# Kernel optimization log

Measured on AMD Instinct MI355X. Metric: run time of the kernel, lower is better.

## Reference

```python
import jax, jax.numpy as jnp
import numpy as np

S = 128      # number of segments
F = 256      # in_features
H = 128      # mlp hidden


def setup_inputs() -> dict:
    key = jax.random.key(0)
    k1, k2, k3 = jax.random.split(key, 3)
    rng = np.random.default_rng(0)
    lengths = rng.integers(1024, 3073, size=S).astype(np.int32)  # ragged segment sizes
    N = int(lengths.sum())  # ~262144 total tokens
    x = jax.random.normal(k1, (N, F), dtype=jnp.float32)
    W1 = jax.random.normal(k2, (F, H), dtype=jnp.float32) * (1.0 / np.sqrt(F))
    b1 = jnp.zeros((H,), dtype=jnp.float32)
    W2 = jax.random.normal(k3, (H, 2), dtype=jnp.float32) * (1.0 / np.sqrt(H))
    b2 = jnp.zeros((2,), dtype=jnp.float32)
    return {"x": x, "lengths": jnp.asarray(lengths), "W1": W1, "b1": b1, "W2": W2, "b2": b2}


def reference(x, lengths, W1, b1, W2, b2):
    N = x.shape[0]
    nseg = lengths.shape[0]
    seg_ids = jnp.repeat(jnp.arange(nseg), lengths, total_repeat_length=N)  # [N]
    offsets = jnp.concatenate([jnp.zeros((1,), lengths.dtype), jnp.cumsum(lengths)[:-1]])
    # position within segment: arange(1, L+1) / L
    pos = (jnp.arange(N) - offsets[seg_ids] + 1).astype(x.dtype)
    Lf = lengths.astype(x.dtype)
    xpos = pos / Lf[seg_ids]  # [N]

    # MLP: Linear -> Tanh -> Linear
    ms = jnp.tanh(x @ W1 + b1) @ W2 + b2  # [N, 2]
    y, z = ms[:, 0], ms[:, 1]

    # per-segment softmax-weighted mean of positions (calc_mean)
    ymax = jax.ops.segment_max(y, seg_ids, num_segments=nseg)
    w = jnp.exp(y - ymax[seg_ids])
    wsum = jax.ops.segment_sum(w, seg_ids, num_segments=nseg)
    means = jax.ops.segment_sum(xpos * w, seg_ids, num_segments=nseg) / wsum  # [S]

    # per-segment softplus(mean(z))
    stds = jax.nn.softplus(jax.ops.segment_sum(z, seg_ids, num_segments=nseg) / Lf)  # [S]

    # normal pdf weights per token
    mu = means[seg_ids]
    sd = stds[seg_ids]
    inv_sqrt_2pi = 1.0 / jnp.sqrt(2.0 * jnp.pi).astype(x.dtype)
    pdf = jnp.exp(-0.5 * ((xpos - mu) / sd) ** 2) * (inv_sqrt_2pi / sd)  # [N]

    # normalize per segment with +0.001 stabilizer
    psum = jax.ops.segment_sum(pdf, seg_ids, num_segments=nseg)
    attn = (pdf / (psum[seg_ids] + 0.001))[:, None]  # [N, 1]

    # attention-weighted sum of features per segment
    out = jax.ops.segment_sum(attn * x, seg_ids, num_segments=nseg)  # [S, F]
    return out, attn
```

## Files before the change

### kernel.cpp

```cpp
#include <hip/hip_runtime.h>
#include <math.h>

#define F 256
#define Hh 128
#define MAXL 3072

typedef short bf16x8 __attribute__((ext_vector_type(8)));
typedef float f32x4 __attribute__((ext_vector_type(4)));
typedef unsigned int uint4v __attribute__((ext_vector_type(4)));

__device__ inline unsigned short f2bf_rne(float f) {
  unsigned u = __float_as_uint(f);
  unsigned r = u + 0x7fff + ((u >> 16) & 1);
  return (unsigned short)(r >> 16);
}
__device__ inline float bf2f(unsigned short h) {
  return __uint_as_float((unsigned)h << 16);
}

__global__ void init_kernel(const int* __restrict__ lengths, int* __restrict__ offsets,
                            float* __restrict__ out, const float* __restrict__ W1,
                            unsigned short* __restrict__ whT, unsigned short* __restrict__ wlT,
                            int S, int outN) {
  int t = blockIdx.x * blockDim.x + threadIdx.x;
  int stride = gridDim.x * blockDim.x;
  for (int i = t; i < outN; i += stride) out[i] = 0.f;
  for (int i = t; i < F * Hh; i += stride) {
    int k = i >> 7, col = i & 127;
    float v = W1[i];
    unsigned short h = f2bf_rne(v);
    unsigned short l = f2bf_rne(v - bf2f(h));
    int dst = (k >> 5) * (128 * 32) + col * 32 + (k & 31);
    whT[dst] = h;
    wlT[dst] = l;
  }
  if (blockIdx.x == 0) {
    __shared__ int buf[256];
    int tid = threadIdx.x;
    int v = (tid < S) ? lengths[tid] : 0;
    buf[tid] = v;
    __syncthreads();
    for (int o = 1; o < 256; o <<= 1) {
      int add = (tid >= o) ? buf[tid - o] : 0;
      __syncthreads();
      buf[tid] += add;
      __syncthreads();
    }
    if (tid < S) offsets[tid] = buf[tid] - v;
    if (tid == S - 1) offsets[S] = buf[tid];
  }
}

__global__ __launch_bounds__(256) void mlp_kernel(
    const float* __restrict__ x,
    const unsigned short* __restrict__ whT, const unsigned short* __restrict__ wlT,
    const float* __restrict__ b1, const float* __restrict__ W2,
    const float* __restrict__ b2, float* __restrict__ yv,
    float* __restrict__ zv, int N) {
  __shared__ float redy[128][2];
  __shared__ float redz[128][2];

  const int t = threadIdx.x;
  const int lane = t & 63;
  const int w = t >> 6;
  const int wr = w >> 1, wc = w & 1;
  const int ln15 = lane & 15, lq = lane >> 4;

  const int row0 = blockIdx.x * 128;

  f32x4 acc[4][4];
#pragma unroll
  for (int i = 0; i < 4; ++i)
#pragma unroll
    for (int j = 0; j < 4; ++j) acc[i][j] = (f32x4){0.f, 0.f, 0.f, 0.f};

  int rowg[4];
  bool rv[4];
#pragma unroll
  for (int rt = 0; rt < 4; ++rt) {
    rowg[rt] = row0 + wr * 64 + rt * 16 + ln15;
    rv[rt] = rowg[rt] < N;
  }
  const int cbase = wc * 64 + ln15;

  for (int kc = 0; kc < 8; ++kc) {
    float4 av0[4], av1[4];
#pragma unroll
    for (int rt = 0; rt < 4; ++rt) {
      av0[rt] = make_float4(0.f, 0.f, 0.f, 0.f);
      av1[rt] = make_float4(0.f, 0.f, 0.f, 0.f);
      if (rv[rt]) {
        const float* p = &x[(size_t)rowg[rt] * F + kc * 32 + lq * 8];
        av0[rt] = *(const float4*)p;
        av1[rt] = *(const float4*)(p + 4);
      }
    }
    bf16x8 bh[4], bl[4];
#pragma unroll
    for (int ct = 0; ct < 4; ++ct) {
      int o = kc * 4096 + (cbase + ct * 16) * 32 + lq * 8;
      bh[ct] = *(const bf16x8*)&whT[o];
      bl[ct] = *(const bf16x8*)&wlT[o];
    }
#pragma unroll
    for (int rt = 0; rt < 4; ++rt) {
      float f[8] = {av0[rt].x, av0[rt].y, av0[rt].z, av0[rt].w,
                    av1[rt].x, av1[rt].y, av1[rt].z, av1[rt].w};
      union { uint4v u; bf16x8 b; } ah, al;
#pragma unroll
      for (int q = 0; q < 4; ++q) {
        unsigned ua = __float_as_uint(f[2 * q]);
        unsigned ub = __float_as_uint(f[2 * q + 1]);
        ah.u[q] = __builtin_amdgcn_perm(ub, ua, 0x07060302u);
        float ra = f[2 * q]     - __uint_as_float(ua & 0xFFFF0000u);
        float rb = f[2 * q + 1] - __uint_as_float(ub & 0xFFFF0000u);
        al.u[q] = __builtin_amdgcn_perm(__float_as_uint(rb), __float_as_uint(ra), 0x07060302u);
      }
#pragma unroll
      for (int ct = 0; ct < 4; ++ct) {
        acc[rt][ct] = __builtin_amdgcn_mfma_f32_16x16x32_bf16(ah.b, bh[ct], acc[rt][ct], 0, 0, 0);
        acc[rt][ct] = __builtin_amdgcn_mfma_f32_16x16x32_bf16(ah.b, bl[ct], acc[rt][ct], 0, 0, 0);
        acc[rt][ct] = __builtin_amdgcn_mfma_f32_16x16x32_bf16(al.b, bh[ct], acc[rt][ct], 0, 0, 0);
      }
    }
  }

  float yp[4][4], zp[4][4];
#pragma unroll
  for (int i = 0; i < 4; ++i)
#pragma unroll
    for (int j = 0; j < 4; ++j) { yp[i][j] = 0.f; zp[i][j] = 0.f; }
#pragma unroll
  for (int ct = 0; ct < 4; ++ct) {
    int c = cbase + ct * 16;
    float b1c = b1[c], wyc = W2[2 * c], wzc = W2[2 * c + 1];
#pragma unroll
    for (int rt = 0; rt < 4; ++rt)
#pragma unroll
      for (int rg = 0; rg < 4; ++rg) {
        float a = acc[rt][ct][rg] + b1c;
        float e = __expf(2.f * a);
        float h = 1.f - __fdividef(2.f, e + 1.f);
        yp[rt][rg] = fmaf(h, wyc, yp[rt][rg]);
        zp[rt][rg] = fmaf(h, wzc, zp[rt][rg]);
      }
  }
#pragma unroll
  for (int rt = 0; rt < 4; ++rt)
#pragma unroll
    for (int rg = 0; rg < 4; ++rg) {
      float vy = yp[rt][rg], vz = zp[rt][rg];
#pragma unroll
      for (int m = 8; m; m >>= 1) {
        vy += __shfl_xor(vy, m);
        vz += __shfl_xor(vz, m);
      }
      if (ln15 == 0) {
        int row = wr * 64 + rt * 16 + lq * 4 + rg;
        redy[row][wc] = vy;
        redz[row][wc] = vz;
      }
    }
  __syncthreads();
  if (t < 128) {
    int g = row0 + t;
    if (g < N) {
      yv[g] = redy[t][0] + redy[t][1] + b2[0];
      zv[g] = redz[t][0] + redz[t][1] + b2[1];
    }
  }
}

__device__ inline float wave_reduce_sum(float v) {
#pragma unroll
  for (int o = 32; o; o >>= 1) v += __shfl_down(v, o);
  return v;
}
__device__ inline float wave_reduce_max(float v) {
#pragma unroll
  for (int o = 32; o; o >>= 1) v = fmaxf(v, __shfl_down(v, o));
  return v;
}

__global__ __launch_bounds__(256) void pool_kernel(
    const float* __restrict__ x,
    const float* __restrict__ yv, const float* __restrict__ zv,
    const int* __restrict__ offsets, const int* __restrict__ lengths,
    float* __restrict__ attn, float* __restrict__ out,
    int nchunks, int S) {
  __shared__ float ybuf[MAXL];
  __shared__ float4 sbuf[4][64];
  __shared__ float redA[4], redB[4], redC[4];

  const int s = S - 1 - blockIdx.y;
  const int c = nchunks - 1 - blockIdx.x;
  const int off = offsets[s], L = lengths[s];
  const int t = threadIdx.x;
  const int lane = t & 63, wid = t >> 6;

  float lmax = -1e30f;
  for (int i = t; i < L; i += 256) {
    float yy = yv[off + i];
    ybuf[i] = yy;
    lmax = fmaxf(lmax, yy);
  }
  lmax = wave_reduce_max(lmax);
  if (lane == 0) redA[wid] = lmax;
  __syncthreads();
  const float ymax = fmaxf(fmaxf(redA[0], redA[1]), fmaxf(redA[2], redA[3]));
  const float invL = 1.f / (float)L;
  __syncthreads();

  float sw = 0.f, smx = 0.f, sz = 0.f;
  for (int i = t; i < L; i += 256) {
    float wgt = __expf(ybuf[i] - ymax);
    float xp = (float)(i + 1) * invL;
    sw += wgt;
    smx = fmaf(xp, wgt, smx);
    sz += zv[off + i];
  }
  sw = wave_reduce_sum(sw);
  smx = wave_reduce_sum(smx);
  sz = wave_reduce_sum(sz);
  if (lane == 0) { redA[wid] = sw; redB[wid] = smx; redC[wid] = sz; }
  __syncthreads();
  const float wsum = (redA[0] + redA[1]) + (redA[2] + redA[3]);
  const float mxs  = (redB[0] + redB[1]) + (redB[2] + redB[3]);
  const float zsum = (redC[0] + redC[1]) + (redC[2] + redC[3]);
  const float mu = mxs / wsum;
  const float tz = zsum * invL;
  const float sd = fmaxf(tz, 0.f) + log1pf(__expf(-fabsf(tz)));
  const float invsd = 1.f / sd;
  const float Cg = 0.3989422804014327f;
  __syncthreads();

  float ps = 0.f;
  for (int i = t; i < L; i += 256) {
    float xp = (float)(i + 1) * invL;
    float u = (xp - mu) * invsd;
    ps += __expf(-0.5f * u * u);
  }
  ps = wave_reduce_sum(ps);
  if (lane == 0) redA[wid] = ps;
  __syncthreads();
  const float psum = ((redA[0] + redA[1]) + (redA[2] + redA[3])) * (Cg * invsd);
  const float scale = (Cg * invsd) / (psum + 0.001f);

  const int i0 = (int)((long long)L * c / nchunks);
  const int i1 = (int)((long long)L * (c + 1) / nchunks);
  for (int i = i0 + t; i < i1; i += 256) {
    float xp = (float)(i + 1) * invL;
    float u = (xp - mu) * invsd;
    attn[off + i] = __expf(-0.5f * u * u) * scale;
  }

  float4 a0 = make_float4(0.f, 0.f, 0.f, 0.f);
  float4 a1 = make_float4(0.f, 0.f, 0.f, 0.f);
  int i = i1 - 1 - wid;
  for (; i - 4 >= i0; i -= 8) {
    float xpa = (float)(i + 1) * invL;
    float ua = (xpa - mu) * invsd;
    float w0 = __expf(-0.5f * ua * ua) * scale;
    float xpb = (float)(i - 3) * invL;
    float ub = (xpb - mu) * invsd;
    float w1 = __expf(-0.5f * ub * ub) * scale;
    float4 v0 = *(const float4*)&x[(size_t)(off + i) * F + lane * 4];
    float4 v1 = *(const float4*)&x[(size_t)(off + i - 4) * F + lane * 4];
    a0.x = fmaf(w0, v0.x, a0.x); a0.y = fmaf(w0, v0.y, a0.y);
    a0.z = fmaf(w0, v0.z, a0.z); a0.w = fmaf(w0, v0.w, a0.w);
    a1.x = fmaf(w1, v1.x, a1.x); a1.y = fmaf(w1, v1.y, a1.y);
    a1.z = fmaf(w1, v1.z, a1.z); a1.w = fmaf(w1, v1.w, a1.w);
  }
  if (i >= i0) {
    float xpa = (float)(i + 1) * invL;
    float ua = (xpa - mu) * invsd;
    float w0 = __expf(-0.5f * ua * ua) * scale;
    float4 v0 = *(const float4*)&x[(size_t)(off + i) * F + lane * 4];
    a0.x = fmaf(w0, v0.x, a0.x); a0.y = fmaf(w0, v0.y, a0.y);
    a0.z = fmaf(w0, v0.z, a0.z); a0.w = fmaf(w0, v0.w, a0.w);
  }
  a0.x += a1.x; a0.y += a1.y; a0.z += a1.z; a0.w += a1.w;
  sbuf[wid][lane] = a0;
  __syncthreads();
  if (wid == 0) {
    float4 r0 = sbuf[0][lane], r1 = sbuf[1][lane];
    float4 r2 = sbuf[2][lane], r3 = sbuf[3][lane];
    float rx = (r0.x + r1.x) + (r2.x + r3.x);
    float ry = (r0.y + r1.y) + (r2.y + r3.y);
    float rz = (r0.z + r1.z) + (r2.z + r3.z);
    float rw = (r0.w + r1.w) + (r2.w + r3.w);
    float* o = &out[s * F + lane * 4];
    atomicAdd(o + 0, rx);
    atomicAdd(o + 1, ry);
    atomicAdd(o + 2, rz);
    atomicAdd(o + 3, rw);
  }
}

extern "C" void kernel_launch(void* const* d_in, const int* in_sizes, int n_in,
                              void* d_out, int out_size, void* d_ws, size_t ws_size,
                              hipStream_t stream) {
  const float* x      = (const float*)d_in[0];
  const int* lengths  = (const int*)d_in[1];
  const float* W1     = (const float*)d_in[2];
  const float* b1     = (const float*)d_in[3];
  const float* W2     = (const float*)d_in[4];
  const float* b2     = (const float*)d_in[5];
  const int S = in_sizes[1];
  const int N = in_sizes[0] / F;

  float* out  = (float*)d_out;
  float* attn = out + (size_t)S * F;

  int*   offsets = (int*)d_ws;
  float* yv = (float*)d_ws + 512;
  float* zv = yv + N;
  unsigned short* whT = (unsigned short*)(zv + N);
  unsigned short* wlT = whT + F * Hh;

  init_kernel<<<64, 256, 0, stream>>>(lengths, offsets, out, W1, whT, wlT, S, S * F);
  mlp_kernel<<<(N + 127) / 128, 256, 0, stream>>>(x, whT, wlT, b1, W2, b2, yv, zv, N);
  pool_kernel<<<dim3(32, S), 256, 0, stream>>>(x, yv, zv, offsets, lengths, attn, out, 32, S);
}
```

Baseline: 459.9 us.

## Halve MLP row tile, double-buffer x loads, and cut pool chunks

Result: slower. 482.6 us (+4.9%).

```diff
diff --git a/kernel.cpp b/kernel.cpp
--- a/kernel.cpp
+++ b/kernel.cpp
@@ -51,14 +51,26 @@
   }
 }
 
+#define LOADX(B, KC) do {                                             \
+    _Pragma("unroll")                                                 \
+    for (int rt = 0; rt < 2; ++rt) {                                  \
+      a0[B][rt] = make_float4(0.f, 0.f, 0.f, 0.f);                    \
+      a1[B][rt] = make_float4(0.f, 0.f, 0.f, 0.f);                    \
+      if (rv[rt]) {                                                   \
+        a0[B][rt] = *(const float4*)(xb[rt] + (KC) * 32);             \
+        a1[B][rt] = *(const float4*)(xb[rt] + (KC) * 32 + 4);         \
+      }                                                               \
+    }                                                                 \
+  } while (0)
+
 __global__ __launch_bounds__(256) void mlp_kernel(
     const float* __restrict__ x,
     const unsigned short* __restrict__ whT, const unsigned short* __restrict__ wlT,
     const float* __restrict__ b1, const float* __restrict__ W2,
     const float* __restrict__ b2, float* __restrict__ yv,
     float* __restrict__ zv, int N) {
-  __shared__ float redy[128][2];
-  __shared__ float redz[128][2];
+  __shared__ float redy[64][2];
+  __shared__ float redz[64][2];
 
   const int t = threadIdx.x;
   const int lane = t & 63;
@@ -66,46 +78,43 @@
   const int wr = w >> 1, wc = w & 1;
   const int ln15 = lane & 15, lq = lane >> 4;
 
-  const int row0 = blockIdx.x * 128;
-
-  f32x4 acc[4][4];
-#pragma unroll
-  for (int i = 0; i < 4; ++i)
+  const int row0 = blockIdx.x * 64;
+
+  f32x4 acc[2][4];
+#pragma unroll
+  for (int i = 0; i < 2; ++i)
 #pragma unroll
     for (int j = 0; j < 4; ++j) acc[i][j] = (f32x4){0.f, 0.f, 0.f, 0.f};
 
-  int rowg[4];
-  bool rv[4];
-#pragma unroll
-  for (int rt = 0; rt < 4; ++rt) {
-    rowg[rt] = row0 + wr * 64 + rt * 16 + ln15;
-    rv[rt] = rowg[rt] < N;
+  bool rv[2];
+  const float* xb[2];
+#pragma unroll
+  for (int rt = 0; rt < 2; ++rt) {
+    int rowg = row0 + wr * 32 + rt * 16 + ln15;
+    rv[rt] = rowg < N;
+    xb[rt] = x + (size_t)rowg * F + lq * 8;
   }
   const int cbase = wc * 64 + ln15;
-
+  const unsigned short* wb = whT + cbase * 32 + lq * 8;
+  const unsigned short* lb = wlT + cbase * 32 + lq * 8;
+
+  float4 a0[2][2], a1[2][2];
+  LOADX(0, 0);
+
+#pragma unroll
   for (int kc = 0; kc < 8; ++kc) {
-    float4 av0[4], av1[4];
-#pragma unroll
-    for (int rt = 0; rt < 4; ++rt) {
-      av0[rt] = make_float4(0.f, 0.f, 0.f, 0.f);
-      av1[rt] = make_float4(0.f, 0.f, 0.f, 0.f);
-      if (rv[rt]) {
-        const float* p = &x[(size_t)rowg[rt] * F + kc * 32 + lq * 8];
-        av0[rt] = *(const float4*)p;
-        av1[rt] = *(const float4*)(p + 4);
-      }
-    }
+    const int cur = kc & 1, nxt = cur ^ 1;
+    if (kc < 7) LOADX(nxt, kc + 1);
     bf16x8 bh[4], bl[4];
 #pragma unroll
     for (int ct = 0; ct < 4; ++ct) {
-      int o = kc * 4096 + (cbase + ct * 16) * 32 + lq * 8;
-      bh[ct] = *(const bf16x8*)&whT[o];
-      bl[ct] = *(const bf16x8*)&wlT[o];
-    }
-#pragma unroll
-    for (int rt = 0; rt < 4; ++rt) {
-      float f[8] = {av0[rt].x, av0[rt].y, av0[rt].z, av0[rt].w,
-                    av1[rt].x, av1[rt].y, av1[rt].z, av1[rt].w};
+      bh[ct] = *(const bf16x8*)(wb + kc * 4096 + ct * 512);
+      bl[ct] = *(const bf16x8*)(lb + kc * 4096 + ct * 512);
+    }
+#pragma unroll
+    for (int rt = 0; rt < 2; ++rt) {
+      float f[8] = {a0[cur][rt].x, a0[cur][rt].y, a0[cur][rt].z, a0[cur][rt].w,
+                    a1[cur][rt].x, a1[cur][rt].y, a1[cur][rt].z, a1[cur][rt].w};
       union { uint4v u; bf16x8 b; } ah, al;
 #pragma unroll
       for (int q = 0; q < 4; ++q) {
@@ -125,9 +134,9 @@
     }
   }
 
-  float yp[4][4], zp[4][4];
-#pragma unroll
-  for (int i = 0; i < 4; ++i)
+  float yp[2][4], zp[2][4];
+#pragma unroll
+  for (int i = 0; i < 2; ++i)
 #pragma unroll
     for (int j = 0; j < 4; ++j) { yp[i][j] = 0.f; zp[i][j] = 0.f; }
 #pragma unroll
@@ -135,7 +144,7 @@
     int c = cbase + ct * 16;
     float b1c = b1[c], wyc = W2[2 * c], wzc = W2[2 * c + 1];
 #pragma unroll
-    for (int rt = 0; rt < 4; ++rt)
+    for (int rt = 0; rt < 2; ++rt)
 #pragma unroll
       for (int rg = 0; rg < 4; ++rg) {
         float a = acc[rt][ct][rg] + b1c;
@@ -146,7 +155,7 @@
       }
   }
 #pragma unroll
-  for (int rt = 0; rt < 4; ++rt)
+  for (int rt = 0; rt < 2; ++rt)
 #pragma unroll
     for (int rg = 0; rg < 4; ++rg) {
       float vy = yp[rt][rg], vz = zp[rt][rg];
@@ -156,13 +165,13 @@
         vz += __shfl_xor(vz, m);
       }
       if (ln15 == 0) {
-        int row = wr * 64 + rt * 16 + lq * 4 + rg;
+        int row = wr * 32 + rt * 16 + lq * 4 + rg;
         redy[row][wc] = vy;
         redz[row][wc] = vz;
       }
     }
   __syncthreads();
-  if (t < 128) {
+  if (t < 64) {
     int g = row0 + t;
     if (g < N) {
       yv[g] = redy[t][0] + redy[t][1] + b2[0];
@@ -170,6 +179,7 @@
     }
   }
 }
+#undef LOADX
 
 __device__ inline float wave_reduce_sum(float v) {
 #pragma unroll
@@ -319,6 +329,6 @@
   unsigned short* wlT = whT + F * Hh;
 
   init_kernel<<<64, 256, 0, stream>>>(lengths, offsets, out, W1, whT, wlT, S, S * F);
-  mlp_kernel<<<(N + 127) / 128, 256, 0, stream>>>(x, whT, wlT, b1, W2, b2, yv, zv, N);
-  pool_kernel<<<dim3(32, S), 256, 0, stream>>>(x, yv, zv, offsets, lengths, attn, out, 32, S);
-}
+  mlp_kernel<<<(N + 63) / 64, 256, 0, stream>>>(x, whT, wlT, b1, W2, b2, yv, zv, N);
+  pool_kernel<<<dim3(8, S), 256, 0, stream>>>(x, yv, zv, offsets, lengths, attn, out, 8, S);
+}
```

## Software-pipeline x loads in MLP kernel and reduce pool chunks

Applied to the files above, without the earlier changes.

Measured after the change: 472.5 us. 1.03x slower.

```diff
diff --git a/kernel.cpp b/kernel.cpp
--- a/kernel.cpp
+++ b/kernel.cpp
@@ -51,6 +51,57 @@
   }
 }
 
+#define LOADP(KC) do {                                                \
+    _Pragma("unroll")                                                 \
+    for (int rt = 0; rt < 2; ++rt) {                                  \
+      pa0[rt] = make_float4(0.f, 0.f, 0.f, 0.f);                      \
+      pa1[rt] = make_float4(0.f, 0.f, 0.f, 0.f);                      \
+      if (rv[rt]) {                                                   \
+        const float* p = xb[rt] + (KC) * 32;                          \
+        pa0[rt] = *(const float4*)p;                                  \
+        pa1[rt] = *(const float4*)(p + 4);                            \
+      }                                                               \
+    }                                                                 \
+  } while (0)
+
+#define LOADQ(KC) do {                                                \
+    _Pragma("unroll")                                                 \
+    for (int rt = 0; rt < 2; ++rt) {                                  \
+      qa0[rt] = make_float4(0.f, 0.f, 0.f, 0.f);                      \
+      qa1[rt] = make_float4(0.f, 0.f, 0.f, 0.f);                      \
+      if (rv[rt + 2]) {                                               \
+        const float* p = xb[rt + 2] + (KC) * 32;                      \
+        qa0[rt] = *(const float4*)p;                                  \
+        qa1[rt] = *(const float4*)(p + 4);                            \
+      }                                                               \
+    }                                                                 \
+  } while (0)
+
+#define SPLIT_MFMA(V0, V1, RT) do {                                   \
+    float f[8] = {V0.x, V0.y, V0.z, V0.w, V1.x, V1.y, V1.z, V1.w};    \
+    union { uint4v u; bf16x8 b; } ah, al;                             \
+    _Pragma("unroll")                                                 \
+    for (int q = 0; q < 4; ++q) {                                     \
+      unsigned ua = __float_as_uint(f[2 * q]);                        \
+      unsigned ub = __float_as_uint(f[2 * q + 1]);                    \
+      ah.u[q] = __builtin_amdgcn_perm(ub, ua, 0x07060302u);           \
+      float ra = f[2 * q]     - __uint_as_float(ua & 0xFFFF0000u);    \
+      float rb = f[2 * q + 1] - __uint_as_float(ub & 0xFFFF0000u);    \
+      al.u[q] = __builtin_amdgcn_perm(__float_as_uint(rb),            \
+                                      __float_as_uint(ra),            \
+                                      0x07060302u);                   \
+    }                                                                 \
+    _Pragma("unroll")                                                 \
+    for (int ct = 0; ct < 4; ++ct) {                                  \
+      acc[RT][ct] = __builtin_amdgcn_mfma_f32_16x16x32_bf16(          \
+          ah.b, bh[ct], acc[RT][ct], 0, 0, 0);                        \
+      acc[RT][ct] = __builtin_amdgcn_mfma_f32_16x16x32_bf16(          \
+          ah.b, bl[ct], acc[RT][ct], 0, 0, 0);                        \
+      acc[RT][ct] = __builtin_amdgcn_mfma_f32_16x16x32_bf16(          \
+          al.b, bh[ct], acc[RT][ct], 0, 0, 0);                        \
+    }                                                                 \
+  } while (0)
+
 __global__ __launch_bounds__(256) void mlp_kernel(
     const float* __restrict__ x,
     const unsigned short* __restrict__ whT, const unsigned short* __restrict__ wlT,
@@ -74,55 +125,36 @@
 #pragma unroll
     for (int j = 0; j < 4; ++j) acc[i][j] = (f32x4){0.f, 0.f, 0.f, 0.f};
 
-  int rowg[4];
   bool rv[4];
+  const float* xb[4];
 #pragma unroll
   for (int rt = 0; rt < 4; ++rt) {
-    rowg[rt] = row0 + wr * 64 + rt * 16 + ln15;
-    rv[rt] = rowg[rt] < N;
+    int rowg = row0 + wr * 64 + rt * 16 + ln15;
+    rv[rt] = rowg < N;
+    xb[rt] = x + (size_t)rowg * F + lq * 8;
   }
   const int cbase = wc * 64 + ln15;
+  const unsigned short* wb = whT + cbase * 32 + lq * 8;
+  const unsigned short* lb = wlT + cbase * 32 + lq * 8;
+
+  float4 pa0[2], pa1[2];
+  float4 qa0[2], qa1[2];
+  LOADP(0);
+  LOADQ(0);
 
   for (int kc = 0; kc < 8; ++kc) {
-    float4 av0[4], av1[4];
-#pragma unroll
-    for (int rt = 0; rt < 4; ++rt) {
-      av0[rt] = make_float4(0.f, 0.f, 0.f, 0.f);
-      av1[rt] = make_float4(0.f, 0.f, 0.f, 0.f);
-      if (rv[rt]) {
-        const float* p = &x[(size_t)rowg[rt] * F + kc * 32 + lq * 8];
-        av0[rt] = *(const float4*)p;
-        av1[rt] = *(const float4*)(p + 4);
-      }
+    bf16x8 bh[4], bl[4];
+#pragma unroll
+    for (int ct = 0; ct < 4; ++ct) {
+      bh[ct] = *(const bf16x8*)(wb + kc * 4096 + ct * 512);
+      bl[ct] = *(const bf16x8*)(lb + kc * 4096 + ct * 512);
     }
-    bf16x8 bh[4], bl[4];
-#pragma unroll
-    for (int ct = 0; ct < 4; ++ct) {
-      int o = kc * 4096 + (cbase + ct * 16) * 32 + lq * 8;
-      bh[ct] = *(const bf16x8*)&whT[o];
-      bl[ct] = *(const bf16x8*)&wlT[o];
-    }
-#pragma unroll
-    for (int rt = 0; rt < 4; ++rt) {
-      float f[8] = {av0[rt].x, av0[rt].y, av0[rt].z, av0[rt].w,
-                    av1[rt].x, av1[rt].y, av1[rt].z, av1[rt].w};
-      union { uint4v u; bf16x8 b; } ah, al;
-#pragma unroll
-      for (int q = 0; q < 4; ++q) {
-        unsigned ua = __float_as_uint(f[2 * q]);
-        unsigned ub = __float_as_uint(f[2 * q + 1]);
-        ah.u[q] = __builtin_amdgcn_perm(ub, ua, 0x07060302u);
-        float ra = f[2 * q]     - __uint_as_float(ua & 0xFFFF0000u);
-        float rb = f[2 * q + 1] - __uint_as_float(ub & 0xFFFF0000u);
-        al.u[q] = __builtin_amdgcn_perm(__float_as_uint(rb), __float_as_uint(ra), 0x07060302u);
-      }
-#pragma unroll
-      for (int ct = 0; ct < 4; ++ct) {
-        acc[rt][ct] = __builtin_amdgcn_mfma_f32_16x16x32_bf16(ah.b, bh[ct], acc[rt][ct], 0, 0, 0);
-        acc[rt][ct] = __builtin_amdgcn_mfma_f32_16x16x32_bf16(ah.b, bl[ct], acc[rt][ct], 0, 0, 0);
-        acc[rt][ct] = __builtin_amdgcn_mfma_f32_16x16x32_bf16(al.b, bh[ct], acc[rt][ct], 0, 0, 0);
-      }
-    }
+    SPLIT_MFMA(pa0[0], pa1[0], 0);
+    SPLIT_MFMA(pa0[1], pa1[1], 1);
+    if (kc < 7) LOADP(kc + 1);
+    SPLIT_MFMA(qa0[0], qa1[0], 2);
+    SPLIT_MFMA(qa0[1], qa1[1], 3);
+    if (kc < 7) LOADQ(kc + 1);
   }
 
   float yp[4][4], zp[4][4];
@@ -170,6 +202,9 @@
     }
   }
 }
+#undef LOADP
+#undef LOADQ
+#undef SPLIT_MFMA
 
 __device__ inline float wave_reduce_sum(float v) {
 #pragma unroll
@@ -320,5 +355,5 @@
 
   init_kernel<<<64, 256, 0, stream>>>(lengths, offsets, out, W1, whT, wlT, S, S * F);
   mlp_kernel<<<(N + 127) / 128, 256, 0, stream>>>(x, whT, wlT, b1, W2, b2, yv, zv, N);
-  pool_kernel<<<dim3(32, S), 256, 0, stream>>>(x, yv, zv, offsets, lengths, attn, out, 32, S);
-}
+  pool_kernel<<<dim3(8, S), 256, 0, stream>>>(x, yv, zv, offsets, lengths, attn, out, 8, S);
+}
```

## Double-buffer x tiles into LDS via async global_load_lds in MLP kernel

Applied to the files above, without the earlier changes.

New measurement: 463.3 us. No clear change (+0.7%).

```diff
diff --git a/kernel.cpp b/kernel.cpp
--- a/kernel.cpp
+++ b/kernel.cpp
@@ -51,12 +51,50 @@
   }
 }
 
+#define STAGE(B, KC) do {                                               \
+    _Pragma("unroll")                                                   \
+    for (int r = 0; r < 4; ++r) {                                       \
+      __builtin_amdgcn_global_load_lds(                                 \
+          (const __attribute__((address_space(1))) unsigned int*)       \
+              (srow[r] + (KC) * 32),                                    \
+          (__attribute__((address_space(3))) unsigned int*)             \
+              (xs + (B) * 4096 + r * 1024 + t * 4),                     \
+          16, 0, 0);                                                    \
+    }                                                                   \
+  } while (0)
+
+#define SPLIT_MFMA(V0, V1, RT) do {                                     \
+    float f[8] = {V0.x, V0.y, V0.z, V0.w, V1.x, V1.y, V1.z, V1.w};      \
+    union { uint4v u; bf16x8 b; } ah, al;                               \
+    _Pragma("unroll")                                                   \
+    for (int q = 0; q < 4; ++q) {                                       \
+      unsigned ua = __float_as_uint(f[2 * q]);                          \
+      unsigned ub = __float_as_uint(f[2 * q + 1]);                      \
+      ah.u[q] = __builtin_amdgcn_perm(ub, ua, 0x07060302u);             \
+      float ra = f[2 * q]     - __uint_as_float(ua & 0xFFFF0000u);      \
+      float rb = f[2 * q + 1] - __uint_as_float(ub & 0xFFFF0000u);      \
+      al.u[q] = __builtin_amdgcn_perm(__float_as_uint(rb),              \
+                                      __float_as_uint(ra),              \
+                                      0x07060302u);                     \
+    }                                                                   \
+    _Pragma("unroll")                                                   \
+    for (int ct = 0; ct < 4; ++ct) {                                    \
+      acc[RT][ct] = __builtin_amdgcn_mfma_f32_16x16x32_bf16(            \
+          ah.b, bh[ct], acc[RT][ct], 0, 0, 0);                          \
+      acc[RT][ct] = __builtin_amdgcn_mfma_f32_16x16x32_bf16(            \
+          ah.b, bl[ct], acc[RT][ct], 0, 0, 0);                          \
+      acc[RT][ct] = __builtin_amdgcn_mfma_f32_16x16x32_bf16(            \
+          al.b, bh[ct], acc[RT][ct], 0, 0, 0);                          \
+    }                                                                   \
+  } while (0)
+
 __global__ __launch_bounds__(256) void mlp_kernel(
     const float* __restrict__ x,
     const unsigned short* __restrict__ whT, const unsigned short* __restrict__ wlT,
     const float* __restrict__ b1, const float* __restrict__ W2,
     const float* __restrict__ b2, float* __restrict__ yv,
     float* __restrict__ zv, int N) {
+  __shared__ float xs[2 * 4096];
   __shared__ float redy[128][2];
   __shared__ float redz[128][2];
 
@@ -74,55 +112,48 @@
 #pragma unroll
     for (int j = 0; j < 4; ++j) acc[i][j] = (f32x4){0.f, 0.f, 0.f, 0.f};
 
-  int rowg[4];
-  bool rv[4];
-#pragma unroll
-  for (int rt = 0; rt < 4; ++rt) {
-    rowg[rt] = row0 + wr * 64 + rt * 16 + ln15;
-    rv[rt] = rowg[rt] < N;
-  }
+  const float* srow[4];
+  {
+    const int rsub = t >> 3;
+    const int swzs = (rsub & 7) << 4;
+    const int scolb = ((t & 7) * 16) ^ swzs;
+#pragma unroll
+    for (int r = 0; r < 4; ++r) {
+      int grow = row0 + r * 32 + rsub;
+      grow = grow < N ? grow : N - 1;
+      srow[r] = x + (size_t)grow * F + (scolb >> 2);
+    }
+  }
+
+  const int row_l = wr * 64 + ln15;
+  const int swzr = (ln15 & 7) << 4;
+  const int p0base = row_l * 128 + ((lq * 32) ^ swzr);
+
   const int cbase = wc * 64 + ln15;
-
+  const unsigned short* wb = whT + cbase * 32 + lq * 8;
+  const unsigned short* lb = wlT + cbase * 32 + lq * 8;
+
+  STAGE(0, 0);
+  __syncthreads();
+
+#pragma unroll
   for (int kc = 0; kc < 8; ++kc) {
-    float4 av0[4], av1[4];
+    if (kc < 7) STAGE((kc + 1) & 1, kc + 1);
+    bf16x8 bh[4], bl[4];
+#pragma unroll
+    for (int ct = 0; ct < 4; ++ct) {
+      bh[ct] = *(const bf16x8*)(wb + kc * 4096 + ct * 512);
+      bl[ct] = *(const bf16x8*)(lb + kc * 4096 + ct * 512);
+    }
+    const char* bufp = (const char*)xs + (kc & 1) * 16384;
 #pragma unroll
     for (int rt = 0; rt < 4; ++rt) {
-      av0[rt] = make_float4(0.f, 0.f, 0.f, 0.f);
-      av1[rt] = make_float4(0.f, 0.f, 0.f, 0.f);
-      if (rv[rt]) {
-        const float* p = &x[(size_t)rowg[rt] * F + kc * 32 + lq * 8];
-        av0[rt] = *(const float4*)p;
-        av1[rt] = *(const float4*)(p + 4);
-      }
-    }
-    bf16x8 bh[4], bl[4];
-#pragma unroll
-    for (int ct = 0; ct < 4; ++ct) {
-      int o = kc * 4096 + (cbase + ct * 16) * 32 + lq * 8;
-      bh[ct] = *(const bf16x8*)&whT[o];
-      bl[ct] = *(const bf16x8*)&wlT[o];
-    }
-#pragma unroll
-    for (int rt = 0; rt < 4; ++rt) {
-      float f[8] = {av0[rt].x, av0[rt].y, av0[rt].z, av0[rt].w,
-                    av1[rt].x, av1[rt].y, av1[rt].z, av1[rt].w};
-      union { uint4v u; bf16x8 b; } ah, al;
-#pragma unroll
-      for (int q = 0; q < 4; ++q) {
-        unsigned ua = __float_as_uint(f[2 * q]);
-        unsigned ub = __float_as_uint(f[2 * q + 1]);
-        ah.u[q] = __builtin_amdgcn_perm(ub, ua, 0x07060302u);
-        float ra = f[2 * q]     - __uint_as_float(ua & 0xFFFF0000u);
-        float rb = f[2 * q + 1] - __uint_as_float(ub & 0xFFFF0000u);
-        al.u[q] = __builtin_amdgcn_perm(__float_as_uint(rb), __float_as_uint(ra), 0x07060302u);
-      }
-#pragma unroll
-      for (int ct = 0; ct < 4; ++ct) {
-        acc[rt][ct] = __builtin_amdgcn_mfma_f32_16x16x32_bf16(ah.b, bh[ct], acc[rt][ct], 0, 0, 0);
-        acc[rt][ct] = __builtin_amdgcn_mfma_f32_16x16x32_bf16(ah.b, bl[ct], acc[rt][ct], 0, 0, 0);
-        acc[rt][ct] = __builtin_amdgcn_mfma_f32_16x16x32_bf16(al.b, bh[ct], acc[rt][ct], 0, 0, 0);
-      }
-    }
+      const int p0 = p0base + rt * 2048;
+      float4 lo = *(const float4*)(bufp + p0);
+      float4 hi = *(const float4*)(bufp + (p0 ^ 16));
+      SPLIT_MFMA(lo, hi, rt);
+    }
+    __syncthreads();
   }
 
   float yp[4][4], zp[4][4];
@@ -170,6 +201,8 @@
     }
   }
 }
+#undef STAGE
+#undef SPLIT_MFMA
 
 __device__ inline float wave_reduce_sum(float v) {
 #pragma unroll
@@ -320,5 +353,5 @@
 
   init_kernel<<<64, 256, 0, stream>>>(lengths, offsets, out, W1, whT, wlT, S, S * F);
   mlp_kernel<<<(N + 127) / 128, 256, 0, stream>>>(x, whT, wlT, b1, W2, b2, yv, zv, N);
-  pool_kernel<<<dim3(32, S), 256, 0, stream>>>(x, yv, zv, offsets, lengths, attn, out, 32, S);
-}
+  pool_kernel<<<dim3(8, S), 256, 0, stream>>>(x, yv, zv, offsets, lengths, attn, out, 8, S);
+}
```
